# Optimization experiments

Hardware: AMD Instinct MI355X
Metric: run time of the kernel (lower is better)

Reference implementation:

```python
import jax, jax.numpy as jnp
import numpy as np

# dims: N batch, D latent, K mixtures, S latent samples, IN_DIM data dim, H hidden
N, D, K, S, IN_DIM, H = 512, 64, 10, 10, 784, 512
LOG2PI = float(np.log(2.0 * np.pi))


def setup_inputs() -> dict:
    key = jax.random.key(0)
    ks = jax.random.split(key, 12)
    rn = lambda k, shp, s=0.05: jax.random.normal(k, shp, jnp.float32) * s
    z = lambda shp: jnp.zeros(shp, jnp.float32)
    return {
        "y": jax.random.normal(ks[0], (N, IN_DIM), jnp.float32),
        "enc_W1": rn(ks[1], (IN_DIM, H)), "enc_b1": z((H,)),
        "enc_Wmu": rn(ks[2], (H, D)), "enc_bmu": z((D,)),
        "enc_Wv": rn(ks[3], (H, D)), "enc_bv": z((D,)),
        "mu_k": rn(ks[4], (K, D), 1.0),
        "L_k_raw": rn(ks[5], (K, D, D), 0.3),
        "pi_k_raw": rn(ks[6], (K,), 1.0),
        "dec_W1": rn(ks[7], (D, H)), "dec_b1": z((H,)),
        "dec_Wmu": rn(ks[8], (H, IN_DIM)), "dec_bmu": z((IN_DIM,)),
        "dec_Wv": rn(ks[9], (H, IN_DIM)), "dec_bv": z((IN_DIM,)),
    }


def _unpack_recognition_gmm(mu_k, L_k_raw, pi_k_raw):
    # tril with softplus-transformed diagonal, P = L L^T, eta2 = -0.5 P
    Lt = jnp.tril(L_k_raw)
    dvals = jax.nn.softplus(jnp.diagonal(Lt, axis1=-2, axis2=-1))  # (K,D)
    eye = jnp.eye(D, dtype=Lt.dtype)
    Lk = Lt * (1.0 - eye) + dvals[:, :, None] * eye
    eta2_phi2 = -0.5 * (Lk @ jnp.swapaxes(Lk, -1, -2))  # (K,D,D)
    pi_phi2 = jax.nn.softmax(pi_k_raw)
    return mu_k, eta2_phi2, pi_phi2


def _svae_forward(y, enc_W1, enc_b1, enc_Wmu, enc_bmu, enc_Wv, enc_bv,
                  mu_k, L_k_raw, pi_k_raw,
                  dec_W1, dec_b1, dec_Wmu, dec_bmu, dec_Wv, dec_bv):
    # --- recognition network: natural-parameter Gaussian potentials ---
    h = jnp.tanh(y @ enc_W1 + enc_b1)
    mu = h @ enc_Wmu + enc_bmu                               # (N,D)
    var = jax.nn.softplus(h @ enc_Wv + enc_bv) + 1e-6        # (N,D)
    eta1_phi1 = mu / var                                     # (N,D)
    eye = jnp.eye(D, dtype=y.dtype)
    eta2_phi1 = (-0.5 / var)[:, None, :] * eye               # (N,D,D) diag

    # --- recognition GMM params ---
    eta1_phi2, eta2_phi2, pi_phi2 = _unpack_recognition_gmm(mu_k, L_k_raw, pi_k_raw)

    # --- compute_log_z_given_y (faithful to original einsums/solves) ---
    eta2_tilde = eta2_phi1[:, None] + eta2_phi2[None]        # (N,K,D,D)
    solved = jnp.linalg.solve(eta2_phi2[None], eta2_tilde)   # eta2_phi2^{-1} eta2_tilde
    w_eta2 = jnp.einsum('nij,nkjl->nkil', eta2_phi1, solved)
    w_eta2 = 0.5 * (w_eta2 + jnp.swapaxes(w_eta2, -1, -2))   # (N,K,D,D)
    solved2 = jnp.linalg.solve(
        eta2_tilde, jnp.broadcast_to(eta1_phi2[None, :, :, None], (1, K, D, 1)))
    w_eta1 = jnp.einsum('nij,nkuv->nkj', eta2_phi1, solved2)  # (N,K,D)

    # gaussian.natural_to_standard: mu = (-2 eta2)^{-1} eta1
    mu_phi1 = jnp.linalg.solve(-2.0 * eta2_phi1, eta1_phi1[:, :, None])[..., 0]  # (N,D)

    # gaussian.log_prob_nat: normalized log responsibilities
    quad = (jnp.einsum('nd,nkd->nk', mu_phi1, w_eta1)
            + jnp.einsum('nd,nkde,ne->nk', mu_phi1, w_eta2, mu_phi1))
    s = jnp.linalg.solve(w_eta2, w_eta1[..., None])[..., 0]   # (N,K,D)
    _, logdet = jnp.linalg.slogdet(-2.0 * w_eta2)             # (N,K)
    logprob = (quad + 0.25 * jnp.einsum('nkd,nkd->nk', w_eta1, s)
               + 0.5 * logdet - 0.5 * D * LOG2PI + jnp.log(pi_phi2)[None, :])
    log_z_given_y = jax.nn.log_softmax(logprob, axis=-1)      # (N,K)

    # --- sample_x_per_comp ---
    inv_sigma = -2.0 * w_eta2                                 # (N,K,D,D) pd
    L = jnp.linalg.cholesky(inv_sigma)
    eps = jax.random.normal(jax.random.key(42), (N, K, D, S), dtype=y.dtype)
    eps = jnp.linalg.solve(jnp.swapaxes(L, -1, -2), eps)
    x_samples = jnp.swapaxes(
        jnp.linalg.solve(inv_sigma, w_eta1[..., None]) + eps, -1, -2)  # (N,K,S,D)

    # --- generative network (standard output: mean, var) ---
    hd = jnp.tanh(x_samples @ dec_W1 + dec_b1)                # (N,K,S,H)
    mean_pred = hd @ dec_Wmu + dec_bmu                        # (N,K,S,IN_DIM)
    var_pred = jax.nn.softplus(hd @ dec_Wv + dec_bv) + 1e-6

    # --- subsample_x: multinomial over mixture responsibilities + gather ---
    zc = jax.random.categorical(jax.random.key(7), log_z_given_y[:, None, :],
                                shape=(N, S))                 # (N,S) int
    x_sub = x_samples[jnp.arange(N)[:, None], zc, jnp.arange(S)[None, :], :]  # (N,S,D)
    x_subsamples = x_sub[:, 0, :]                             # (N,D)

    return mean_pred, var_pred, x_subsamples, log_z_given_y


def reference(y, enc_W1, enc_b1, enc_Wmu, enc_bmu, enc_Wv, enc_bv,
              mu_k, L_k_raw, pi_k_raw,
              dec_W1, dec_b1, dec_Wmu, dec_bmu, dec_Wv, dec_bv):
    return _svae_forward(y, enc_W1, enc_b1, enc_Wmu, enc_bmu, enc_Wv, enc_bv,
                         mu_k, L_k_raw, pi_k_raw,
                         dec_W1, dec_b1, dec_Wmu, dec_bmu, dec_Wv, dec_bv)
```

## Files before the change

### kernel.cpp

```cpp
#include <hip/hip_runtime.h>
#include <math.h>
#include <stdint.h>

#define N_ 512
#define D_ 64
#define K_ 10
#define S_ 10
#define INDIM_ 784
#define H_ 512
#define DP1 (D_ + 1)

typedef __attribute__((ext_vector_type(8))) short short8v;
typedef __attribute__((ext_vector_type(4))) float f32x4;

__device__ __forceinline__ uint32_t rotl32(uint32_t v, int r) { return (v << r) | (v >> (32 - r)); }

__device__ __forceinline__ void threefry2x32(uint32_t k0, uint32_t k1,
                                             uint32_t x0, uint32_t x1,
                                             uint32_t& o0, uint32_t& o1) {
  uint32_t k2 = k0 ^ k1 ^ 0x1BD11BDAu;
  x0 += k0; x1 += k1;
#define TFR(r) { x0 += x1; x1 = rotl32(x1, r); x1 ^= x0; }
  TFR(13) TFR(15) TFR(26) TFR(6)
  x0 += k1; x1 += k2 + 1u;
  TFR(17) TFR(29) TFR(16) TFR(24)
  x0 += k2; x1 += k0 + 2u;
  TFR(13) TFR(15) TFR(26) TFR(6)
  x0 += k0; x1 += k1 + 3u;
  TFR(17) TFR(29) TFR(16) TFR(24)
  x0 += k1; x1 += k2 + 4u;
  TFR(13) TFR(15) TFR(26) TFR(6)
  x0 += k2; x1 += k0 + 5u;
#undef TFR
  o0 = x0; o1 = x1;
}

__device__ __forceinline__ uint32_t jax_bits32(uint32_t k0, uint32_t k1, uint32_t idx) {
  uint32_t o0, o1; threefry2x32(k0, k1, 0u, idx, o0, o1);
  return o0 ^ o1;
}

__device__ __forceinline__ float bits_to_u01(uint32_t bits) {
  return __uint_as_float((bits >> 9) | 0x3F800000u) - 1.0f;
}

__device__ __forceinline__ float erfinv_f32(float x) {
  float w = -log1pf(-x * x);
  float p;
  if (w < 5.0f) {
    w = w - 2.5f;
    p = 2.81022636e-08f;
    p = fmaf(p, w, 3.43273939e-07f);
    p = fmaf(p, w, -3.5233877e-06f);
    p = fmaf(p, w, -4.39150654e-06f);
    p = fmaf(p, w, 0.00021858087f);
    p = fmaf(p, w, -0.00125372503f);
    p = fmaf(p, w, -0.00417768164f);
    p = fmaf(p, w, 0.246640727f);
    p = fmaf(p, w, 1.50140941f);
  } else {
    w = sqrtf(w) - 3.0f;
    p = -0.000200214257f;
    p = fmaf(p, w, 0.000100950558f);
    p = fmaf(p, w, 0.00134934322f);
    p = fmaf(p, w, -0.00367342844f);
    p = fmaf(p, w, 0.00573950773f);
    p = fmaf(p, w, -0.0076224613f);
    p = fmaf(p, w, 0.00943887047f);
    p = fmaf(p, w, 1.00167406f);
    p = fmaf(p, w, 2.83297682f);
  }
  return p * x;
}

__device__ __forceinline__ float jax_normal_f32(uint32_t k0, uint32_t k1, uint32_t idx) {
  uint32_t bits = jax_bits32(k0, k1, idx);
  float u = bits_to_u01(bits);
  const float lo = -0.99999994f;
  float v = u * (1.0f - lo) + lo;
  v = fmaxf(lo, v);
  return 1.41421356f * erfinv_f32(v);
}

__device__ __forceinline__ float jax_gumbel_f32(uint32_t k0, uint32_t k1, uint32_t idx) {
  uint32_t bits = jax_bits32(k0, k1, idx);
  float u = bits_to_u01(bits);
  const float tiny = 1.17549435e-38f;
  float v = u * (1.0f - tiny) + tiny;
  v = fmaxf(tiny, v);
  return -logf(-logf(v));
}

__device__ __forceinline__ float sp32(float x) { return fmaxf(x, 0.f) + log1pf(expf(-fabsf(x))); }
__device__ __forceinline__ float sp32cr(float x) {
  double xd = (double)x;
  return (float)(fmax(xd, 0.0) + log1p(exp(-fabs(xd))));
}
__device__ __forceinline__ double sp64(double x) { return fmax(x, 0.0) + log1p(exp(-fabs(x))); }

__device__ __forceinline__ float fast_sp(float x) {
  float e = __expf(-fabsf(x));
  return fmaxf(x, 0.f) + __logf(1.0f + e);
}
__device__ __forceinline__ float fast_tanh(float x) {
  float xc = fminf(fmaxf(2.0f * x, -30.0f), 30.0f);
  float e = __expf(xc);
  float r = __builtin_amdgcn_rcpf(e + 1.0f);
  return fmaf(-2.0f, r, 1.0f);
}

__device__ __forceinline__ ushort bf16rne(float f) {
  uint32_t u = __float_as_uint(f);
  uint32_t r = (u + 0x7FFFu + ((u >> 16) & 1u)) >> 16;
  return (ushort)r;
}
__device__ __forceinline__ float bf2f(ushort b) { return __uint_as_float(((uint32_t)b) << 16); }

__global__ __launch_bounds__(256) void k_all1(
    const float* __restrict__ y, const float* __restrict__ eW1, const float* __restrict__ eb1,
    const float* __restrict__ Wmu, const float* __restrict__ bmu,
    const float* __restrict__ Wv, const float* __restrict__ bv,
    double* __restrict__ mu, double* __restrict__ dvec,
    float* __restrict__ d32, float* __restrict__ muph,
    const float* __restrict__ dW1, const float* __restrict__ dWmu, const float* __restrict__ dWv,
    ushort* __restrict__ hF,
    const float* __restrict__ Lraw, const float* __restrict__ piraw, const float* __restrict__ muk,
    double* __restrict__ iJout, double* __restrict__ gko, double* __restrict__ logpi,
    float* __restrict__ J32g, float* __restrict__ LU32g, int* __restrict__ pivg) {
  __shared__ union SM1 {
    struct { double hs[512]; float mu32s[64]; float var32s[64]; } e;
    struct { float Lk[64][DP1]; double dg[64]; double Li[64][DP1]; } g;
    struct { float Lk[64][DP1]; float A[64][DP1]; } u;
  } sm;
  int b = blockIdx.x, t = threadIdx.x;

  if (b < 512) {
    int n = b;
    const float* yr = y + n * INDIM_;
    double a0 = 0.0, a1 = 0.0;
    for (int d = 0; d < INDIM_; ++d) {
      double yv = (double)yr[d];
      a0 += yv * (double)eW1[d * H_ + t];
      a1 += yv * (double)eW1[d * H_ + t + 256];
    }
    sm.e.hs[t] = tanh(a0 + (double)eb1[t]);
    sm.e.hs[t + 256] = tanh(a1 + (double)eb1[t + 256]);
    __syncthreads();
    int c = t & 63;
    if (t < 128) {
      const float* Wsel = (t < 64) ? Wmu : Wv;
      double acc = 0.0;
      for (int q = 0; q < H_; ++q) acc += sm.e.hs[q] * (double)Wsel[q * D_ + c];
      if (t < 64) {
        double m = acc + (double)bmu[c];
        mu[n * D_ + c] = m;
        sm.e.mu32s[c] = (float)m;
      } else {
        double a = acc + (double)bv[c];
        double var = sp64(a) + 1e-6;
        dvec[n * D_ + c] = -0.5 / var;
        float var32 = sp32cr((float)a) + 1e-6f;
        sm.e.var32s[c] = var32;
        d32[n * D_ + c] = (-0.5f) / var32;
      }
    }
    __syncthreads();
    if (t < 64) {
      float var32 = sm.e.var32s[c];
      float dd = (-0.5f) / var32;
      float eta1 = sm.e.mu32s[c] / var32;
      float neg2d = -2.0f * dd;
      muph[n * D_ + c] = eta1 / neg2d;
    }
  } else if (b < 920) {
    int chunk = (b - 512) * 4 + (t >> 6);
    int l = t & 63;
    if (chunk < 1632) {
      int lr = l & 15, lg = l >> 4;
      const float* src; int C, ct, ks; ushort* dst;
      if (chunk < 64)       { src = dW1;  C = 512; ct = chunk >> 1;  ks = chunk & 1;
                              dst = hF + chunk * 512; }
      else if (chunk < 848) { int c2 = chunk - 64;  src = dWmu; C = 784; ct = c2 / 16; ks = c2 % 16;
                              dst = hF + 32768 + c2 * 512; }
      else                  { int c2 = chunk - 848; src = dWv;  C = 784; ct = c2 / 16; ks = c2 % 16;
                              dst = hF + 434176 + c2 * 512; }
      ushort vals[8];
#pragma unroll
      for (int e = 0; e < 8; ++e)
        vals[e] = bf16rne(src[(ks * 32 + lg * 8 + e) * C + ct * 16 + lr]);
      *(short8v*)(dst + l * 8) = *(short8v*)vals;
    }
  } else if (b < 930) {
    int k = b - 920, i = t;
    const float* Lr = Lraw + k * D_ * D_;
    if (t < 64) {
      for (int j = 0; j < i; ++j) sm.g.Lk[i][j] = Lr[i * D_ + j];
      sm.g.dg[i] = sp64((double)Lr[i * D_ + i]);
    }
    __syncthreads();
#define LKD(r, c) ((c) < (r) ? (double)sm.g.Lk[r][c] : sm.g.dg[r])
    if (t < 64) {
      int j = i;
      sm.g.Li[j][j] = 1.0 / sm.g.dg[j];
      for (int r = j + 1; r < D_; ++r) {
        double s = 0.0;
        for (int m = j; m < r; ++m) s += LKD(r, m) * sm.g.Li[m][j];
        sm.g.Li[r][j] = -s / sm.g.dg[r];
      }
    }
    __syncthreads();
    if (t < 64) {
      for (int j = 0; j < D_; ++j) {
        int m0 = max(i, j);
        double s = 0.0;
        for (int m = m0; m < D_; ++m) s += sm.g.Li[m][i] * sm.g.Li[m][j];
        iJout[k * D_ * D_ + i * D_ + j] = -2.0 * s;
      }
      double rv = (double)muk[k * D_ + i];
      for (int j = 0; j < D_; ++j) {
        double xj = __shfl(rv, j, 64) / sm.g.dg[j];
        if (i == j) rv = xj;
        else if (i > j) rv -= (double)sm.g.Lk[i][j] * xj;
      }
      for (int j = D_ - 1; j >= 0; --j) {
        double xj = __shfl(rv, j, 64) / sm.g.dg[j];
        if (i == j) rv = xj;
        else if (i < j) rv -= (double)sm.g.Lk[j][i] * xj;
      }
      gko[k * D_ + i] = 2.0 * rv;
    }
#undef LKD
    if (k == 0 && t == 0) {
      double m = (double)piraw[0];
      for (int q = 1; q < K_; ++q) m = fmax(m, (double)piraw[q]);
      double ss = 0.0;
      for (int q = 0; q < K_; ++q) ss += exp((double)piraw[q] - m);
      double lse = m + log(ss);
      for (int q = 0; q < K_; ++q) logpi[q] = (double)piraw[q] - lse;
    }
  } else {
    int k = b - 930, i = t;
    const float* Lr = Lraw + k * D_ * D_;
    if (t < 64) {
      for (int j = 0; j < D_; ++j)
        sm.u.Lk[i][j] = (j < i) ? Lr[i * D_ + j] : ((j == i) ? sp32cr(Lr[i * D_ + i]) : 0.0f);
    }
    __syncthreads();
    if (t < 64) {
      for (int j = 0; j < D_; ++j) {
        float s = 0.0f;
        for (int q = 0; q < D_; ++q) s = fmaf(sm.u.Lk[i][q], sm.u.Lk[j][q], s);
        sm.u.A[i][j] = -0.5f * s;
      }
    }
    __syncthreads();
    if (t < 64)
      for (int r = 0; r < D_; ++r)
        J32g[k * 4096 + r * 64 + i] = sm.u.A[r][i];
    int mypiv = i;
    for (int j = 0; j < D_; ++j) {
      __syncthreads();
      if (t < 64) {
        float v = (i >= j) ? fabsf(sm.u.A[i][j]) : -1.0f;
        int ix = i;
        for (int off = 32; off > 0; off >>= 1) {
          float v2 = __shfl_xor(v, off, 64);
          int i2 = __shfl_xor(ix, off, 64);
          if (v2 > v || (v2 == v && i2 < ix)) { v = v2; ix = i2; }
        }
        int p = ix;
        if (i == j) mypiv = p;
        if (p != j) { float tmp = sm.u.A[j][i]; sm.u.A[j][i] = sm.u.A[p][i]; sm.u.A[p][i] = tmp; }
      }
      __syncthreads();
      if (t < 64 && i > j) {
        float rec = 1.0f / sm.u.A[j][j];
        float x = sm.u.A[i][j] * rec;
        sm.u.A[i][j] = x;
        int l = j + 1;
        for (; l + 7 < D_; l += 8) {
          float p0 = sm.u.A[j][l+0], p1 = sm.u.A[j][l+1], p2 = sm.u.A[j][l+2], p3 = sm.u.A[j][l+3];
          float p4 = sm.u.A[j][l+4], p5 = sm.u.A[j][l+5], p6 = sm.u.A[j][l+6], p7 = sm.u.A[j][l+7];
          float o0 = sm.u.A[i][l+0], o1 = sm.u.A[i][l+1], o2 = sm.u.A[i][l+2], o3 = sm.u.A[i][l+3];
          float o4 = sm.u.A[i][l+4], o5 = sm.u.A[i][l+5], o6 = sm.u.A[i][l+6], o7 = sm.u.A[i][l+7];
          o0 = fmaf(x, -p0, o0); o1 = fmaf(x, -p1, o1);
          o2 = fmaf(x, -p2, o2); o3 = fmaf(x, -p3, o3);
          o4 = fmaf(x, -p4, o4); o5 = fmaf(x, -p5, o5);
          o6 = fmaf(x, -p6, o6); o7 = fmaf(x, -p7, o7);
          sm.u.A[i][l+0] = o0; sm.u.A[i][l+1] = o1; sm.u.A[i][l+2] = o2; sm.u.A[i][l+3] = o3;
          sm.u.A[i][l+4] = o4; sm.u.A[i][l+5] = o5; sm.u.A[i][l+6] = o6; sm.u.A[i][l+7] = o7;
        }
        for (; l < D_; ++l) sm.u.A[i][l] = fmaf(x, -sm.u.A[j][l], sm.u.A[i][l]);
      }
    }
    __syncthreads();
    if (t < 64) {
      for (int r = 0; r < D_; ++r)
        LU32g[k * 4096 + r * 64 + i] = sm.u.A[r][i];
      pivg[k * D_ + i] = mypiv;
    }
  }
}

__global__ __launch_bounds__(64) void k_all3(
    const double* __restrict__ dvec, const double* __restrict__ mu,
    const double* __restrict__ gk, const double* __restrict__ iJg,
    double* __restrict__ parts, float* __restrict__ xs,
    const float* __restrict__ J32g, const float* __restrict__ LU32g,
    const int* __restrict__ pivg, const float* __restrict__ d32g,
    const float* __restrict__ muphg, double* __restrict__ quadg) {
  __shared__ union SM3 {
    struct { float LUs[64][DP1]; float dsh[64]; float mph[64]; int pshare[64]; double red[64]; } q;
    struct { float Sp[2080]; } p;
  } sm;
  int b = blockIdx.x;

  if (b < 5120) {
    int nk = b;
    int n = nk / K_, k = nk - n * K_;
    int i = threadIdx.x;
    float* Sp = sm.p.Sp;
    int Ti = (i * (i + 1)) >> 1;

    double dnd = dvec[n * 64 + i];
    float dn = (float)dnd;
    double mn = mu[n * 64 + i];
    const double* iJ = iJg + k * 4096;

    float linv = 0.f, ljj = 1.f;
    float pj = (float)iJ[i];
    for (int j = 0; j < 64; ++j) {
      float nx = (j + 1 < 64) ? (float)iJ[(j + 1) * 64 + i] : 0.f;
      float dj = __shfl(dn, j, 64);
      float v = -(dn * pj * dj);
      if (i == j) v -= dn;
      int Tj = (j * (j + 1)) >> 1;
      float a0 = 0.f, a1 = 0.f, a2 = 0.f, a3 = 0.f;
      int q = 0;
      for (; q + 3 < j; q += 4) {
        a0 = fmaf(Sp[Ti + q],     Sp[Tj + q],     a0);
        a1 = fmaf(Sp[Ti + q + 1], Sp[Tj + q + 1], a1);
        a2 = fmaf(Sp[Ti + q + 2], Sp[Tj + q + 2], a2);
        a3 = fmaf(Sp[Ti + q + 3], Sp[Tj + q + 3], a3);
      }
      for (; q < j; ++q) a0 = fmaf(Sp[Ti + q], Sp[Tj + q], a0);
      v -= ((a0 + a1) + (a2 + a3));
      float sj = __shfl(v, j, 64);
      float s_ = sqrtf(fmaxf(sj, 1e-30f));
      float lc = 1.0f / s_;
      float li = (i == j) ? s_ : v * lc;
      if (i >= j) Sp[Ti + j] = li;
      if (i == j) { linv = lc; ljj = s_; }
      pj = nx;
      __syncthreads();
    }

    float rv = (-dn) * (float)gk[k * 64 + i];
    float uv = dn;
    for (int j = 0; j < 64; ++j) {
      float xz = __shfl(rv * linv, j, 64);
      float xu = __shfl(uv * linv, j, 64);
      float lij = (i > j) ? Sp[Ti + j] : 0.f;
      if (i == j) { rv = xz; uv = xu; }
      else { rv = fmaf(-lij, xz, rv); uv = fmaf(-lij, xu, uv); }
    }
    for (int j = 63; j >= 0; --j) {
      float xz = __shfl(rv * linv, j, 64);
      float xu = __shfl(uv * linv, j, 64);
      float lij = (i < j) ? Sp[((j * (j + 1)) >> 1) + i] : 0.f;
      if (i == j) { rv = xz; uv = xu; }
      else { rv = fmaf(-lij, xz, rv); uv = fmaf(-lij, xu, uv); }
    }
    double zsum = (double)rv;
    for (int o = 32; o > 0; o >>= 1) zsum += __shfl_xor(zsum, o, 64);
    double s_nk = -zsum;
    double w1 = s_nk * dnd;
    float tvf = (float)s_nk * uv;
    double dmw = mn * w1;
    for (int o = 32; o > 0; o >>= 1) dmw += __shfl_xor(dmw, o, 64);
    double dwt = w1 * (double)tvf;
    for (int o = 32; o > 0; o >>= 1) dwt += __shfl_xor(dwt, o, 64);
    double sl = log((double)ljj);
    for (int o = 32; o > 0; o >>= 1) sl += __shfl_xor(sl, o, 64);
    if (i == 0) {
      double* pp = parts + nk * 4;
      pp[0] = dmw; pp[1] = dwt; pp[2] = sl;
    }

    float rr[S_];
    {
      uint32_t base = (uint32_t)((nk * 64 + i) * S_);
#pragma unroll
      for (int s = 0; s < S_; ++s)
        rr[s] = jax_normal_f32(0u, 42u, base + s);
    }
    for (int q = 63; q >= 0; --q) {
      float lq = (i < q) ? Sp[((q * (q + 1)) >> 1) + i] : 0.f;
#pragma unroll
      for (int s = 0; s < S_; ++s) {
        float rq = __shfl(rr[s] * linv, q, 64);
        if (i == q) rr[s] = rq;
        else rr[s] = fmaf(-lq, rq, rr[s]);
      }
    }
    float xm = 0.5f * tvf;
#pragma unroll
    for (int s = 0; s < S_; ++s)
      xs[(nk * S_ + s) * 64 + i] = fmaf(0.70710678f, rr[s], xm);
  } else {
    int nk = b - 5120;
    int n = nk / K_, k = nk - n * K_;
    int tj = threadIdx.x;
    for (int r = 0; r < D_; ++r) sm.q.LUs[r][tj] = LU32g[k * 4096 + r * 64 + tj];
    sm.q.dsh[tj] = d32g[n * 64 + tj];
    sm.q.mph[tj] = muphg[n * 64 + tj];
    int pv = pivg[k * 64 + tj];
    int perm = tj;
    for (int j = 0; j < 64; ++j) {
      int pj = __shfl(pv, j, 64);
      int vj = __shfl(perm, j, 64);
      int vp = __shfl(perm, pj, 64);
      if (tj == j) perm = vp;
      else if (tj == pj) perm = vj;
    }
    sm.q.pshare[tj] = perm;
    __syncthreads();
    float Tc[64];
#pragma unroll
    for (int i2 = 0; i2 < 64; ++i2) {
      int pr = sm.q.pshare[i2];
      float v = J32g[k * 4096 + pr * 64 + tj];
      if (pr == tj) v = v + sm.q.dsh[tj];
      Tc[i2] = v;
    }
#pragma unroll
    for (int r = 0; r < 64; ++r) {
      float x = Tc[r];
#pragma unroll
      for (int i2 = r + 1; i2 < 64; ++i2)
        Tc[i2] = fmaf(sm.q.LUs[i2][r], -x, Tc[i2]);
    }
#pragma unroll
    for (int r = 63; r >= 0; --r) {
      float x = Tc[r] / sm.q.LUs[r][r];
      Tc[r] = x;
#pragma unroll
      for (int i2 = 0; i2 < r; ++i2)
        Tc[i2] = fmaf(sm.q.LUs[i2][r], -x, Tc[i2]);
    }
    __syncthreads();
#pragma unroll
    for (int i2 = 0; i2 < 64; ++i2) sm.q.LUs[i2][tj] = Tc[i2];
    __syncthreads();
    double part = 0.0;
#pragma unroll
    for (int d2 = 0; d2 < 64; ++d2) {
      float a = sm.q.dsh[d2] * Tc[d2];
      float bq = sm.q.dsh[tj] * sm.q.LUs[tj][d2];
      float w = 0.5f * (a + bq);
      float t1 = sm.q.mph[d2] * w;
      float t2 = t1 * sm.q.mph[tj];
      part += (double)t2;
    }
    sm.q.red[tj] = part; __syncthreads();
    for (int off = 32; off > 0; off >>= 1) {
      if (tj < off) sm.q.red[tj] += sm.q.red[tj + off];
      __syncthreads();
    }
    if (tj == 0) quadg[nk] = sm.q.red[0];
  }
}

__global__ __launch_bounds__(256) void k_all4(
    const float* __restrict__ xs,
    const ushort* __restrict__ W1F, const ushort* __restrict__ WmuF, const ushort* __restrict__ WvF,
    const float* __restrict__ b1, const float* __restrict__ bmu, const float* __restrict__ bvv,
    float* __restrict__ outm, float* __restrict__ outv,
    const double* __restrict__ parts, const double* __restrict__ quadg,
    const double* __restrict__ logpi,
    float* __restrict__ outz, float* __restrict__ outx) {
  __shared__ __align__(16) union SM4 {
    ushort hdF[32768];
    struct { double lz[K_]; int zc; } s;
  } sm;
  int b = blockIdx.x, t = threadIdx.x;

  if (b < 800) {
    int w = t >> 6, l = t & 63;
    int lr = l & 15, lg = l >> 4;
    int row0 = b * 64;
    int wrow0 = row0 + w * 16;

    short8v xhi[2], xlo[2];
    {
      const float* xrow = xs + (size_t)(wrow0 + lr) * 64 + lg * 8;
#pragma unroll
      for (int ks = 0; ks < 2; ++ks) {
        ushort hi[8], lo[8];
#pragma unroll
        for (int e = 0; e < 8; ++e) {
          float xv = xrow[ks * 32 + e];
          ushort h16 = bf16rne(xv);
          hi[e] = h16;
          lo[e] = bf16rne(xv - bf2f(h16));
        }
        xhi[ks] = *(short8v*)hi;
        xlo[ks] = *(short8v*)lo;
      }
    }

    const short8v* W1v = (const short8v*)W1F;
#pragma unroll 4
    for (int ct = 0; ct < 32; ++ct) {
      f32x4 acc = {0.f, 0.f, 0.f, 0.f};
      short8v b0 = W1v[(ct * 2 + 0) * 64 + l];
      short8v b1v = W1v[(ct * 2 + 1) * 64 + l];
      acc = __builtin_amdgcn_mfma_f32_16x16x32_bf16(xhi[0], b0, acc, 0, 0, 0);
      acc = __builtin_amdgcn_mfma_f32_16x16x32_bf16(xlo[0], b0, acc, 0, 0, 0);
      acc = __builtin_amdgcn_mfma_f32_16x16x32_bf16(xhi[1], b1v, acc, 0, 0, 0);
      acc = __builtin_amdgcn_mfma_f32_16x16x32_bf16(xlo[1], b1v, acc, 0, 0, 0);
      int c = ct * 16 + lr;
      float bb = b1[c];
      int ks = ct >> 1;
      int blk = ((ct & 1) << 1) | (lr >> 3);
      int eo = lr & 7;
#pragma unroll
      for (int r = 0; r < 4; ++r) {
        int l2 = (lg * 4 + r) + 16 * blk;
        sm.hdF[(((w * 16 + ks) * 64) + l2) * 8 + eo] = bf16rne(fast_tanh(acc[r] + bb));
      }
    }
    __syncthreads();

    const short8v* hdv = (const short8v*)sm.hdF;
    const short8v* Wmv = (const short8v*)WmuF;
    const short8v* Wvv = (const short8v*)WvF;
    for (int ci = w; ci < 49; ci += 4) {
      f32x4 aM[4], aV[4];
#pragma unroll
      for (int rg = 0; rg < 4; ++rg) {
        aM[rg] = (f32x4){0.f, 0.f, 0.f, 0.f};
        aV[rg] = (f32x4){0.f, 0.f, 0.f, 0.f};
      }
#pragma unroll 4
      for (int ks = 0; ks < 16; ++ks) {
        short8v bm = Wmv[(ci * 16 + ks) * 64 + l];
        short8v bv = Wvv[(ci * 16 + ks) * 64 + l];
#pragma unroll
        for (int rg = 0; rg < 4; ++rg) {
          short8v ha = hdv[(rg * 16 + ks) * 64 + l];
          aM[rg] = __builtin_amdgcn_mfma_f32_16x16x32_bf16(ha, bm, aM[rg], 0, 0, 0);
          aV[rg] = __builtin_amdgcn_mfma_f32_16x16x32_bf16(ha, bv, aV[rg], 0, 0, 0);
        }
      }
      int c = ci * 16 + lr;
      float bm_ = bmu[c], bv_ = bvv[c];
#pragma unroll
      for (int rg = 0; rg < 4; ++rg) {
        int rbase = (row0 + rg * 16 + lg * 4) * INDIM_ + c;
#pragma unroll
        for (int r = 0; r < 4; ++r) {
          int o = rbase + r * INDIM_;
          outm[o] = aM[rg][r] + bm_;
          outv[o] = fast_sp(aV[rg][r] + bv_) + 1e-6f;
        }
      }
    }
  } else {
    int n = b - 800;
    if (t == 0) {
      double lp[K_];
      double m = -1e300;
      for (int q = 0; q < K_; ++q) {
        const double* pp = parts + (n * K_ + q) * 4;
        double v = pp[0] + quadg[n * K_ + q];
        v = v - 0.25 * pp[1];
        v = v + 32.0 * 0.6931471805599453;
        v = v + pp[2];
        v = v - 32.0 * 1.8378770664093453;
        v = v + logpi[q];
        lp[q] = v;
        m = fmax(m, v);
      }
      double ss = 0.0;
      for (int q = 0; q < K_; ++q) ss += exp(lp[q] - m);
      double lsum = log(ss);
      float best = -INFINITY; int bi = 0;
      for (int q = 0; q < K_; ++q) {
        double l = (lp[q] - m) - lsum;
        sm.s.lz[q] = l;
        float g = jax_gumbel_f32(0u, 7u, (uint32_t)(n * 100 + q));
        float sc = g + (float)l;
        if (sc > best) { best = sc; bi = q; }
      }
      sm.s.zc = bi;
    }
    __syncthreads();
    if (t < K_) outz[n * K_ + t] = (float)sm.s.lz[t];
    if (t < 64) outx[n * D_ + t] = xs[(n * K_ + sm.s.zc) * S_ * D_ + t];
  }
}

extern "C" void kernel_launch(void* const* d_in, const int* in_sizes, int n_in,
                              void* d_out, int out_size, void* d_ws, size_t ws_size,
                              hipStream_t stream) {
  const float* y     = (const float*)d_in[0];
  const float* eW1   = (const float*)d_in[1];
  const float* eb1   = (const float*)d_in[2];
  const float* eWmu  = (const float*)d_in[3];
  const float* ebmu  = (const float*)d_in[4];
  const float* eWv   = (const float*)d_in[5];
  const float* ebv   = (const float*)d_in[6];
  const float* muk   = (const float*)d_in[7];
  const float* Lraw  = (const float*)d_in[8];
  const float* piraw = (const float*)d_in[9];
  const float* dW1   = (const float*)d_in[10];
  const float* db1   = (const float*)d_in[11];
  const float* dWmu  = (const float*)d_in[12];
  const float* dbmu  = (const float*)d_in[13];
  const float* dWv   = (const float*)d_in[14];
  const float* dbv   = (const float*)d_in[15];

  double* W      = (double*)d_ws;
  double* h      = W;
  double* mu     = W + 262144;
  double* dvec   = W + 294912;
  double* gk     = W + 327680;
  double* parts  = W + 328704;
  double* iJ     = W + 368640;
  double* logpi  = W + 409600;
  double* quadg  = W + 414736;
  double* base2  = W + 419856;
  float*  xs     = (float*)base2;
  float*  J32    = xs + 3276800;
  float*  LU32   = J32 + 40960;
  float*  d32    = LU32 + 40960;
  float*  muph   = d32 + 32768;
  int*    piv    = (int*)(muph + 32768);

  ushort* hF   = (ushort*)h;
  ushort* W1F  = hF;
  ushort* WmuF = hF + 32768;
  ushort* WvF  = hF + 434176;

  float* outm = (float*)d_out;
  float* outv = outm + 40140800;
  float* outx = outm + 80281600;
  float* outz = outm + 80314368;

  k_all1<<<940, 256, 0, stream>>>(y, eW1, eb1, eWmu, ebmu, eWv, ebv,
                                  mu, dvec, d32, muph,
                                  dW1, dWmu, dWv, hF,
                                  Lraw, piraw, muk, iJ, gk, logpi,
                                  J32, LU32, piv);
  k_all3<<<10240, 64, 0, stream>>>(dvec, mu, gk, iJ, parts, xs,
                                   J32, LU32, piv, d32, muph, quadg);
  k_all4<<<1312, 256, 0, stream>>>(xs, W1F, WmuF, WvF, db1, dbmu, dbv,
                                   outm, outv, parts, quadg, logpi, outz, outx);
}
```

Baseline: 677.8 us.

## Pack two (n,k) items per block in k_all3 and share LU factor load

```diff
diff --git a/kernel.cpp b/kernel.cpp
--- a/kernel.cpp
+++ b/kernel.cpp
@@ -302,7 +302,7 @@
   }
 }
 
-__global__ __launch_bounds__(64) void k_all3(
+__global__ __launch_bounds__(128) void k_all3(
     const double* __restrict__ dvec, const double* __restrict__ mu,
     const double* __restrict__ gk, const double* __restrict__ iJg,
     double* __restrict__ parts, float* __restrict__ xs,
@@ -310,16 +310,18 @@
     const int* __restrict__ pivg, const float* __restrict__ d32g,
     const float* __restrict__ muphg, double* __restrict__ quadg) {
   __shared__ union SM3 {
-    struct { float LUs[64][DP1]; float dsh[64]; float mph[64]; int pshare[64]; double red[64]; } q;
-    struct { float Sp[2080]; } p;
+    struct { float LUs[64][DP1]; int pshare[64]; float dsh[2][64]; float mph[2][64]; } q;
+    struct { float Sp[2][2080]; } p;
   } sm;
   int b = blockIdx.x;
-
-  if (b < 5120) {
-    int nk = b;
+  int wv = threadIdx.x >> 6;
+  int lane = threadIdx.x & 63;
+
+  if (b < 2560) {
+    int nk = b * 2 + wv;
     int n = nk / K_, k = nk - n * K_;
-    int i = threadIdx.x;
-    float* Sp = sm.p.Sp;
+    int i = lane;
+    float* Sp = sm.p.Sp[wv];
     int Ti = (i * (i + 1)) >> 1;
 
     double dnd = dvec[n * 64 + i];
@@ -408,29 +410,36 @@
     for (int s = 0; s < S_; ++s)
       xs[(nk * S_ + s) * 64 + i] = fmaf(0.70710678f, rr[s], xm);
   } else {
-    int nk = b - 5120;
-    int n = nk / K_, k = nk - n * K_;
-    int tj = threadIdx.x;
-    for (int r = 0; r < D_; ++r) sm.q.LUs[r][tj] = LU32g[k * 4096 + r * 64 + tj];
-    sm.q.dsh[tj] = d32g[n * 64 + tj];
-    sm.q.mph[tj] = muphg[n * 64 + tj];
-    int pv = pivg[k * 64 + tj];
-    int perm = tj;
-    for (int j = 0; j < 64; ++j) {
-      int pj = __shfl(pv, j, 64);
-      int vj = __shfl(perm, j, 64);
-      int vp = __shfl(perm, pj, 64);
-      if (tj == j) perm = vp;
-      else if (tj == pj) perm = vj;
-    }
-    sm.q.pshare[tj] = perm;
+    int b2 = b - 2560;
+    int k = b2 % K_;
+    int npair = b2 / K_;
+    int n = npair * 2 + wv;
+    int nk = n * K_ + k;
+    int tj = lane;
+
+    for (int r = wv; r < 64; r += 2)
+      sm.q.LUs[r][tj] = LU32g[k * 4096 + r * 64 + tj];
+    sm.q.dsh[wv][tj] = d32g[n * 64 + tj];
+    sm.q.mph[wv][tj] = muphg[n * 64 + tj];
+    if (wv == 0) {
+      int pv = pivg[k * 64 + tj];
+      int perm = tj;
+      for (int j = 0; j < 64; ++j) {
+        int pj = __shfl(pv, j, 64);
+        int vj = __shfl(perm, j, 64);
+        int vp = __shfl(perm, pj, 64);
+        if (tj == j) perm = vp;
+        else if (tj == pj) perm = vj;
+      }
+      sm.q.pshare[tj] = perm;
+    }
     __syncthreads();
     float Tc[64];
 #pragma unroll
     for (int i2 = 0; i2 < 64; ++i2) {
       int pr = sm.q.pshare[i2];
       float v = J32g[k * 4096 + pr * 64 + tj];
-      if (pr == tj) v = v + sm.q.dsh[tj];
+      if (pr == tj) v = v + sm.q.dsh[wv][tj];
       Tc[i2] = v;
     }
 #pragma unroll
@@ -449,25 +458,47 @@
         Tc[i2] = fmaf(sm.q.LUs[i2][r], -x, Tc[i2]);
     }
     __syncthreads();
-#pragma unroll
-    for (int i2 = 0; i2 < 64; ++i2) sm.q.LUs[i2][tj] = Tc[i2];
-    __syncthreads();
-    double part = 0.0;
-#pragma unroll
-    for (int d2 = 0; d2 < 64; ++d2) {
-      float a = sm.q.dsh[d2] * Tc[d2];
-      float bq = sm.q.dsh[tj] * sm.q.LUs[tj][d2];
-      float w = 0.5f * (a + bq);
-      float t1 = sm.q.mph[d2] * w;
-      float t2 = t1 * sm.q.mph[tj];
-      part += (double)t2;
-    }
-    sm.q.red[tj] = part; __syncthreads();
-    for (int off = 32; off > 0; off >>= 1) {
-      if (tj < off) sm.q.red[tj] += sm.q.red[tj + off];
-      __syncthreads();
-    }
-    if (tj == 0) quadg[nk] = sm.q.red[0];
+    if (wv == 0) {
+#pragma unroll
+      for (int i2 = 0; i2 < 64; ++i2) sm.q.LUs[i2][tj] = Tc[i2];
+    }
+    __syncthreads();
+    if (wv == 0) {
+      double part = 0.0;
+#pragma unroll
+      for (int d2 = 0; d2 < 64; ++d2) {
+        float a = sm.q.dsh[0][d2] * Tc[d2];
+        float bq = sm.q.dsh[0][tj] * sm.q.LUs[tj][d2];
+        float w = 0.5f * (a + bq);
+        float t1 = sm.q.mph[0][d2] * w;
+        float t2 = t1 * sm.q.mph[0][tj];
+        part += (double)t2;
+      }
+      for (int off = 32; off > 0; off >>= 1)
+        part += __shfl_xor(part, off, 64);
+      if (tj == 0) quadg[nk] = part;
+    }
+    __syncthreads();
+    if (wv == 1) {
+#pragma unroll
+      for (int i2 = 0; i2 < 64; ++i2) sm.q.LUs[i2][tj] = Tc[i2];
+    }
+    __syncthreads();
+    if (wv == 1) {
+      double part = 0.0;
+#pragma unroll
+      for (int d2 = 0; d2 < 64; ++d2) {
+        float a = sm.q.dsh[1][d2] * Tc[d2];
+        float bq = sm.q.dsh[1][tj] * sm.q.LUs[tj][d2];
+        float w = 0.5f * (a + bq);
+        float t1 = sm.q.mph[1][d2] * w;
+        float t2 = t1 * sm.q.mph[1][tj];
+        part += (double)t2;
+      }
+      for (int off = 32; off > 0; off >>= 1)
+        part += __shfl_xor(part, off, 64);
+      if (tj == 0) quadg[nk] = part;
+    }
   }
 }
 
@@ -653,7 +684,7 @@
                                   dW1, dWmu, dWv, hF,
                                   Lraw, piraw, muk, iJ, gk, logpi,
                                   J32, LU32, piv);
-  k_all3<<<10240, 64, 0, stream>>>(dvec, mu, gk, iJ, parts, xs,
+  k_all3<<<5120, 128, 0, stream>>>(dvec, mu, gk, iJ, parts, xs,
                                    J32, LU32, piv, d32, muph, quadg);
   k_all4<<<1312, 256, 0, stream>>>(xs, W1F, WmuF, WvF, db1, dbmu, dbv,
                                    outm, outv, parts, quadg, logpi, outz, outx);
```

Result: slower. 700.9 us (+3.4%).
